# Kernel optimization log

Measured on AMD Instinct MI355X. Metric: run time of the kernel, lower is better.

Reference implementation:

```python
import jax, jax.numpy as jnp
import numpy as np

QC = 13        # quantum_channel
NQ = 12        # qubits per patch circuit
LAYERS12 = 3   # num_layer for FQConv ansatz
LAYERS4 = 4    # layers for the 4-qubit basic ansatz
GROUPS = 10
DIM = 40       # 3*QC + 1 channels
B = 1024
TDIM = 128
EPS = 1e-6     # flax GroupNorm default epsilon
TWO_PI = 2.0 * float(np.pi)


def _take2(s, ax):
    return jnp.take(s, 0, axis=ax), jnp.take(s, 1, axis=ax)


def init_state(n, N):
    # |0...0> state, shape (N, 2, 2, ..., 2); wire w lives on axis w+1
    s = jnp.zeros((N, 2 ** n), jnp.complex64).at[:, 0].set(1.0)
    return s.reshape((N,) + (2,) * n)


def apply_rx(state, theta, w):
    # RX(theta) = [[c, -i s], [-i s, c]], c=cos(theta/2), s=sin(theta/2)
    ax = w + 1
    theta = jnp.asarray(theta, jnp.float32)
    c = jnp.cos(0.5 * theta)
    s = jnp.sin(0.5 * theta)
    if theta.ndim > 0:  # per-sample angles (data embedding)
        sh = (-1,) + (1,) * (state.ndim - 2)
        c = c.reshape(sh)
        s = s.reshape(sh)
    c = c.astype(state.dtype)
    js = (1j * s).astype(state.dtype)
    s0, s1 = _take2(state, ax)
    return jnp.stack([c * s0 - js * s1, c * s1 - js * s0], axis=ax)


def apply_cnot(state, c, t):
    ca = c + 1
    ta = t + 1 if t < c else t  # target axis inside the control=1 slice
    s0, s1 = _take2(state, ca)
    return jnp.stack([s0, jnp.flip(s1, axis=ta)], axis=ca)


def apply_crz(state, theta, c, t):
    # CRZ = diag(1, 1, e^{-i theta/2}, e^{+i theta/2})
    ca = c + 1
    ta = t + 1 if t < c else t
    s0, s1 = _take2(state, ca)
    t0, t1 = _take2(s1, ta)
    em = jnp.exp(-0.5j * theta).astype(state.dtype)
    ep = jnp.exp(0.5j * theta).astype(state.dtype)
    s1 = jnp.stack([em * t0, ep * t1], axis=ta)
    return jnp.stack([s0, s1], axis=ca)


def apply_crx(state, theta, c, t):
    # controlled RX on target when control = 1
    ca = c + 1
    ta = t + 1 if t < c else t
    s0, s1 = _take2(state, ca)
    t0, t1 = _take2(s1, ta)
    ch = jnp.cos(0.5 * theta).astype(state.dtype)
    js = (1j * jnp.sin(0.5 * theta)).astype(state.dtype)
    s1 = jnp.stack([ch * t0 - js * t1, ch * t1 - js * t0], axis=ta)
    return jnp.stack([s0, s1], axis=ca)


def expvals_z(state, n):
    # <Z_w> = P(bit_w = 0) - P(bit_w = 1)
    p = jnp.real(state * jnp.conj(state))
    zs = []
    for w in range(n):
        axes = tuple(a for a in range(1, n + 1) if a != w + 1)
        q = p.sum(axis=axes)  # (N, 2)
        zs.append(q[:, 0] - q[:, 1])
    return jnp.stack(zs, axis=-1)  # (N, n)


def fqconv_layer(state, th):
    # zip(range(11,-1,-4), range(12)) -> i in (11,7,3), j in (0,1,2)
    for j, i in enumerate((11, 7, 3)):
        w1 = [i - 3, i - 2, i - 1, i] + [(i + k) % NQ for k in (1, 2, 3, 4)]
        tj = th[8 * j: 8 * (j + 1)]
        for bi, bj in zip(range(3, -1, -1), range(4)):  # block_C: CRZ
            state = apply_crz(state, TWO_PI * tj[bj], w1[bi + 4], w1[bi])
        for bi, bj in zip(range(3, -1, -1), range(4)):  # block_D: CRX
            state = apply_crx(state, TWO_PI * tj[4 + bj], w1[bi + 4], w1[bi])
    return state


def circuit12(x, theta):
    # x: (N, 12) angles; theta: (72,)
    state = init_state(NQ, x.shape[0])
    for w in range(NQ):  # AngleEmbedding, rotation='X'
        state = apply_rx(state, x[:, w], w)
    for l in range(LAYERS12):
        state = fqconv_layer(state, theta[24 * l: 24 * (l + 1)])
    return expvals_z(state, NQ)


def circuit4(x, theta):
    # Basic_ansatz, 4 qubits, 4 layers, 4 params/layer
    state = init_state(4, x.shape[0])
    for w in range(4):
        state = apply_rx(state, x[:, w], w)
    for l in range(LAYERS4):
        for w in range(4):
            state = apply_rx(state, theta[4 * l + w], w)
        for w in range(3):
            state = apply_cnot(state, w, w + 1)
        state = apply_cnot(state, 3, 0)
    return expvals_z(state, 4)


def run12_all(y, params, circ):
    # scan over the QC per-channel circuits (same structure, different params)
    def body(carry, xp):
        yy, th = xp
        return carry, circ(yy, th)
    _, zs = jax.lax.scan(body, None, (y, params))
    return zs  # (QC, N, 12)


def group_norm(h, scale, bias):
    Bn, H, W, C = h.shape
    g = h.reshape(Bn, H, W, GROUPS, C // GROUPS)
    mu = g.mean(axis=(1, 2, 4), keepdims=True)
    var = g.var(axis=(1, 2, 4), keepdims=True)
    g = (g - mu) * jax.lax.rsqrt(var + EPS)
    return g.reshape(Bn, H, W, C) * scale + bias


def forward(x, time_emb, qparams12, qparams4, gn0_scale, gn0_bias,
            gn1_scale, gn1_bias, time_w, time_b, circ12=circuit12):
    Bn = x.shape[0]

    def qpass(inp, p12_block):
        # per-channel 12-qubit circuits on 2x2x3 patches
        y = jnp.stack([inp[..., 3 * i:3 * (i + 1)].reshape(-1, 12) for i in range(QC)], 0)
        z = run12_all(y, p12_block, circ12)                      # (QC, Bn, 12)
        h1 = jnp.moveaxis(z.reshape(QC, Bn, 2, 2, 3), 0, -2).reshape(Bn, 2, 2, 3 * QC)
        # NOTE: faithful to the source, BOTH passes use circuit/params[-2]
        h4 = circuit4(inp[..., 3 * QC:].reshape(-1, 4), qparams4[0]).reshape(Bn, 2, 2, 1)
        return jnp.concatenate([h1, h4], axis=-1)                 # (Bn, 2, 2, 40)

    h = qpass(x, qparams12[:QC])
    h = group_norm(h, gn0_scale, gn0_bias)
    t = jax.nn.swish(time_emb) @ time_w + time_b                  # (Bn, 2*DIM)
    scale, shift = jnp.split(t[:, None, None, :], 2, axis=-1)
    h = jax.nn.swish(h * (1.0 + scale) + shift)
    h = qpass(h, qparams12[QC:])
    h = jax.nn.swish(group_norm(h, gn1_scale, gn1_bias))
    return x + h  # C == dim, so no res_conv


def setup_inputs() -> dict:
    key = jax.random.key(0)
    ks = jax.random.split(key, 5)
    return {
        "x": jax.random.normal(ks[0], (B, 2, 2, DIM), jnp.float32),
        "time_emb": jax.random.normal(ks[1], (B, TDIM), jnp.float32),
        "qparams12": jax.random.uniform(ks[2], (2 * QC, 24 * LAYERS12), jnp.float32),
        "qparams4": jax.random.uniform(ks[3], (2, 16), jnp.float32),
        "gn0_scale": jnp.ones((DIM,), jnp.float32),
        "gn0_bias": jnp.zeros((DIM,), jnp.float32),
        "gn1_scale": jnp.ones((DIM,), jnp.float32),
        "gn1_bias": jnp.zeros((DIM,), jnp.float32),
        "time_w": jax.random.normal(ks[4], (TDIM, 2 * DIM), jnp.float32) * (TDIM ** -0.5),
        "time_b": jnp.zeros((2 * DIM,), jnp.float32),
    }


def reference(x, time_emb, qparams12, qparams4, gn0_scale, gn0_bias,
              gn1_scale, gn1_bias, time_w, time_b):
    return forward(x, time_emb, qparams12, qparams4, gn0_scale, gn0_bias,
                   gn1_scale, gn1_bias, time_w, time_b)
```

## Files before the change

### kernel.cpp

```cpp
#include <hip/hip_runtime.h>
#include <math.h>


#define PI_F 3.14159265358979323846f

typedef float f2 __attribute__((ext_vector_type(2)));

__device__ __forceinline__ f2 shfl2(f2 v, int mask)
{
    f2 r;
    r[0] = __shfl_xor(v[0], mask, 64);
    r[1] = __shfl_xor(v[1], mask, 64);
    return r;
}

template<int CB>
__device__ __forceinline__ void crz_ctrlj(float cg, float ss, f2* R, f2* I)
{
#pragma unroll
    for (int j = 0; j < 16; ++j) {
        if (!((j >> CB) & 1)) continue;
        f2 r = R[j], im = I[j];
        R[j] = cg * r - ss * im;
        I[j] = cg * im + ss * r;
    }
}

__device__ __forceinline__ void crz_pairhi_t4(float cg, float sg, f2* R, f2* I)
{
    const f2 mrv = {1.0f, cg};
#pragma unroll
    for (int j = 0; j < 16; ++j) {
        f2 miv = {0.0f, (j & 8) ? sg : -sg};
        f2 r = R[j], im = I[j];
        R[j] = mrv * r - miv * im;
        I[j] = mrv * im + miv * r;
    }
}

__device__ __forceinline__ void crx_pair(float cg, float sg, f2* R, f2* I)
{
#pragma unroll
    for (int j = 0; j < 16; ++j) {
        f2 r = R[j], im = I[j];
        f2 rs = __builtin_shufflevector(r, r, 1, 0);
        f2 is = __builtin_shufflevector(im, im, 1, 0);
        R[j] = cg * r + sg * is;
        I[j] = cg * im - sg * rs;
    }
}

template<int M>
__device__ __forceinline__ void crx_elem(float cg, float sg, f2* R, f2* I)
{
#pragma unroll
    for (int j = 0; j < 16; ++j) {
        if (j & M) continue;
        const int p = j | M;
        f2 r0 = R[j], i0 = I[j], r1 = R[p], i1 = I[p];
        R[j] = cg * r0 + sg * i1;  I[j] = cg * i0 - sg * r1;
        R[p] = cg * r1 + sg * i0;  I[p] = cg * i1 - sg * r0;
    }
}

__device__ __forceinline__ void crx_pairhi_t4(float cg, float sg, f2* R, f2* I)
{
    const f2 cgv = {1.0f, cg};
    const f2 sgv = {0.0f, sg};
#pragma unroll
    for (int j = 0; j < 8; ++j) {
        const int p = j + 8;
        f2 r0 = R[j], i0 = I[j], r1 = R[p], i1 = I[p];
        R[j] = cgv * r0 + sgv * i1;  I[j] = cgv * i0 - sgv * r1;
        R[p] = cgv * r1 + sgv * i0;  I[p] = cgv * i1 - sgv * r0;
    }
}

template<int CB, int LT>
__device__ __forceinline__ void crx_shj(float cg, float sg, f2* R, f2* I)
{
#pragma unroll
    for (int j = 0; j < 16; ++j) {
        if (!((j >> CB) & 1)) continue;
        f2 br = shfl2(R[j], 1 << LT);
        f2 bi = shfl2(I[j], 1 << LT);
        f2 r = R[j], im = I[j];
        R[j] = cg * r + sg * bi;
        I[j] = cg * im - sg * br;
    }
}

template<int LT>
__device__ __forceinline__ void crx_perm_allv(float cg, float sg, f2* R, f2* I)
{
#pragma unroll
    for (int j = 0; j < 16; ++j) {
        float a0 = R[j][0], b0 = I[j][0];
        float a1 = R[j][1], b1 = I[j][1];
        if constexpr (LT == 4) {
            asm("v_permlane16_swap_b32 %0, %1\n\t"
                "v_permlane16_swap_b32 %1, %0" : "+v"(a0), "+v"(b0));
            asm("v_permlane16_swap_b32 %0, %1\n\t"
                "v_permlane16_swap_b32 %1, %0" : "+v"(a1), "+v"(b1));
        } else {
            asm("v_permlane32_swap_b32 %0, %1\n\t"
                "v_permlane32_swap_b32 %1, %0" : "+v"(a0), "+v"(b0));
            asm("v_permlane32_swap_b32 %0, %1\n\t"
                "v_permlane32_swap_b32 %1, %0" : "+v"(a1), "+v"(b1));
        }
        f2 A = {a0, a1}, Bv = {b0, b1};
        f2 r = R[j], im = I[j];
        R[j] = cg * r + sg * A;
        I[j] = cg * im - sg * Bv;
    }
}

__device__ __forceinline__ void crz_g0_fused(const float* a, f2* R, f2* I,
                                             int lane, int wv)
{
    float gr[4], gi[4];
#pragma unroll
    for (int m = 0; m < 4; ++m) {
        bool cb = (m < 3) ? ((lane >> (3 + m)) & 1) : (wv != 0);
        gr[m] = cb ? a[2 * m]     : 1.0f;
        gi[m] = cb ? a[2 * m + 1] : 0.0f;
    }
    float u0 = gr[1] * gr[0], v0 = gi[1] * gi[0];
    float w0 = gr[1] * gi[0], z0 = gi[1] * gr[0];
    float p01r[2] = { u0 - v0, u0 + v0 };
    float p01i[2] = { -(w0 + z0), w0 - z0 };
    float u1 = gr[3] * gr[2], v1 = gi[3] * gi[2];
    float w1 = gr[3] * gi[2], z1 = gi[3] * gr[2];
    float p23r[2] = { u1 - v1, u1 + v1 };
    float p23i[2] = { -(w1 + z1), w1 - z1 };

    float Mr[8], Mi[8];
#pragma unroll
    for (int t = 0; t < 8; ++t) {
        const int t10 = t & 3, t2 = (t >> 2) & 1;
        float br = (t10 == 0 || t10 == 3) ? p01r[0] : p01r[1];
        float bi = (t10 == 0) ? p01i[0] : (t10 == 1) ? p01i[1]
                 : (t10 == 2) ? -p01i[1] : -p01i[0];
        float ar = p23r[t2], ai = p23i[t2];
        Mr[t] = ar * br - ai * bi;
        Mi[t] = ar * bi + ai * br;
    }
#pragma unroll
    for (int j = 0; j < 16; ++j) {
        const int jj = j & 7;
        f2 mr, mi;
        if (jj < 4) {
            mr = f2{ Mr[2 * jj],      Mr[2 * jj + 1] };
            mi = f2{ Mi[2 * jj],      Mi[2 * jj + 1] };
        } else {
            mr = f2{ Mr[15 - 2 * jj], Mr[14 - 2 * jj] };
            mi = f2{ -Mi[15 - 2 * jj], -Mi[14 - 2 * jj] };
        }
        f2 r = R[j], im = I[j];
        R[j] = mr * r - mi * im;
        I[j] = mr * im + mi * r;
    }
}

__device__ __forceinline__ void crz_g2_fused(const float* a, f2* R, f2* I,
                                             int lane, int wv)
{
    float s0p = ((lane >> 3) & 1) ? a[1] : -a[1];
    bool cb1 = lane & 1;
    float sg1 = ((lane >> 4) & 1) ? a[3] : -a[3];
    float g1r = cb1 ? a[2] : 1.0f, g1i = cb1 ? sg1 : 0.0f;
    bool cb2 = (lane >> 1) & 1;
    float sg2 = ((lane >> 5) & 1) ? a[5] : -a[5];
    float g2r = cb2 ? a[4] : 1.0f, g2i = cb2 ? sg2 : 0.0f;
    bool cb3 = (lane >> 2) & 1;
    float sg3 = wv ? a[7] : -a[7];
    float g3r = cb3 ? a[6] : 1.0f, g3i = cb3 ? sg3 : 0.0f;
    float t12r = g1r * g2r - g1i * g2i, t12i = g1r * g2i + g1i * g2r;
    float Sr  = t12r * g3r - t12i * g3i;
    float Si_ = t12r * g3i + t12i * g3r;
    float T1r = Sr * a[0] - Si_ * s0p;
    float T1i = Sr * s0p + Si_ * a[0];
#pragma unroll
    for (int j = 0; j < 16; ++j) {
        float tr = (j & 8) ? T1r : Sr;
        float ti = (j & 8) ? T1i : Si_;
        f2 r = R[j], im = I[j];
        R[j] = tr * r - ti * im;
        I[j] = tr * im + ti * r;
    }
}

__global__ void __launch_bounds__(256, 2)
qpass12_kernel(const float* __restrict__ inp, const float* __restrict__ cs,
               float* __restrict__ outp)
{
    __shared__ f2 xbufv[2 * 2 * 32 * 33];
    float* xbuff = reinterpret_cast<float*>(xbufv);
    const int tid  = threadIdx.x;
    const int simL = tid >> 7;
    const int ts   = tid & 127;
    const int wv   = ts >> 6;
    const int lane = ts & 63;
    const int sim  = blockIdx.x * 2 + simL;
    const int ci = sim % 13;
    const int b  = sim / 13;
    const float* csc = cs + ci * 144;
    const int ibase = b * 160 + ci * 3;

    float cw[12], sw[12];
#pragma unroll
    for (int w = 0; w < 12; ++w) {
        float x = inp[ibase + (w / 3) * 40 + (w % 3)];
        __sincosf(0.5f * x, &sw[w], &cw[w]);
    }

    float pref = wv ? sw[0] : cw[0];
#pragma unroll
    for (int w = 1; w < 7; ++w)
        pref *= ((lane >> (6 - w)) & 1) ? sw[w] : cw[w];

    float fb[8], eb[4];
#pragma unroll
    for (int t = 0; t < 8; ++t)
        fb[t] = ((t & 1) ? sw[11] : cw[11]) * ((t & 2) ? sw[10] : cw[10]) *
                ((t & 4) ? sw[9] : cw[9]);
#pragma unroll
    for (int t = 0; t < 4; ++t)
        eb[t] = pref * ((t & 1) ? sw[8] : cw[8]) * ((t & 2) ? sw[7] : cw[7]);
    f2 fbv[4];
#pragma unroll
    for (int t = 0; t < 4; ++t)
        fbv[t] = f2{ fb[2 * t], fb[2 * t + 1] };

    const int pl = (__popc(lane) + wv) & 3;
    float oa = (pl == 0) ? 1.0f : (pl == 2) ? -1.0f : 0.0f;
    float ob = (pl == 1) ? -1.0f : (pl == 3) ? 1.0f : 0.0f;

    f2 R[16], I[16];
#pragma unroll
    for (int j = 0; j < 16; ++j) {
        f2 v2 = eb[j >> 2] * fbv[j & 3];
        const int q0 = ((j & 1) + ((j >> 1) & 1) + ((j >> 2) & 1) + ((j >> 3) & 1)) & 3;
        const int q1 = (q0 + 1) & 3;
        const float c0l = (q0 == 0) ? oa : (q0 == 1) ? ob : (q0 == 2) ? -oa : -ob;
        const float c1l = (q0 == 0) ? ob : (q0 == 1) ? -oa : (q0 == 2) ? -ob : oa;
        const float c0h = (q1 == 0) ? oa : (q1 == 1) ? ob : (q1 == 2) ? -oa : -ob;
        const float c1h = (q1 == 0) ? ob : (q1 == 1) ? -oa : (q1 == 2) ? -ob : oa;
        R[j] = f2{ v2[0] * c0l, v2[1] * c0h };
        I[j] = f2{ v2[0] * c1l, v2[1] * c1h };
    }

    const bool act = (lane >> 2) & 1;
    const int  ai  = ((lane >> 3) << 2) | (lane & 3);
    f2* xw = &xbufv[(((simL << 1) | wv) * 32 + ai) * 33];
    f2* xr = &xbufv[(((simL << 1) | (wv ^ 1)) * 32 + ai) * 33];

#pragma unroll 1
    for (int l = 0; l < 3; ++l) {
        const float* a = csc + l * 48;

        crz_g0_fused(a, R, I, lane, wv);
        { bool cb = (lane >> 3) & 1;
          crx_pair(cb ? a[ 8] : 1.0f, cb ? a[ 9] : 0.0f, R, I); }
        { bool cb = (lane >> 4) & 1;
          crx_elem<1>(cb ? a[10] : 1.0f, cb ? a[11] : 0.0f, R, I); }
        { bool cb = (lane >> 5) & 1;
          crx_elem<2>(cb ? a[12] : 1.0f, cb ? a[13] : 0.0f, R, I); }
        { bool cb = wv != 0;
          crx_elem<4>(cb ? a[14] : 1.0f, cb ? a[15] : 0.0f, R, I); }

        crz_pairhi_t4(a[16], a[17], R, I);
        { float ss = (lane & 1)        ? a[19] : -a[19]; crz_ctrlj<0>(a[18], ss, R, I); }
        { float ss = ((lane >> 1) & 1) ? a[21] : -a[21]; crz_ctrlj<1>(a[20], ss, R, I); }
        { float ss = ((lane >> 2) & 1) ? a[23] : -a[23]; crz_ctrlj<2>(a[22], ss, R, I); }
        crx_pairhi_t4(a[24], a[25], R, I);
        crx_shj<0, 0>(a[26], a[27], R, I);
        crx_shj<1, 1>(a[28], a[29], R, I);
        crx_shj<2, 2>(a[30], a[31], R, I);

        crz_g2_fused(a + 32, R, I, lane, wv);
        crx_shj<3, 3>(a[40], a[41], R, I);
        { bool cb = lane & 1;
          crx_perm_allv<4>(cb ? a[42] : 1.0f, cb ? a[43] : 0.0f, R, I); }
        { bool cb = (lane >> 1) & 1;
          crx_perm_allv<5>(cb ? a[44] : 1.0f, cb ? a[45] : 0.0f, R, I); }
        __syncthreads();
        if (act) {
#pragma unroll
            for (int j = 0; j < 16; ++j) {
                xw[j]      = R[j];
                xw[16 + j] = I[j];
            }
        }
        __syncthreads();
        if (act) {
            float cg = a[46], sg = a[47];
#pragma unroll
            for (int j = 0; j < 16; ++j) {
                f2 br = xr[j], bi = xr[16 + j];
                f2 r = R[j], im = I[j];
                R[j] = cg * r + sg * bi;
                I[j] = cg * im - sg * br;
            }
        }
    }

    f2 accT = {0.0f, 0.0f}, acc7 = {0.0f, 0.0f}, acc8 = {0.0f, 0.0f};
    f2 acc9 = {0.0f, 0.0f}, acc10 = {0.0f, 0.0f};
#pragma unroll
    for (int j = 0; j < 16; ++j) {
        f2 p = R[j] * R[j] + I[j] * I[j];
        accT += p;
        if (j & 8) acc7 -= p; else acc7 += p;
        if (j & 4) acc8 -= p; else acc8 += p;
        if (j & 2) acc9 -= p; else acc9 += p;
        if (j & 1) acc10 -= p; else acc10 += p;
    }
    float total = accT[0] + accT[1];
    float v12[12];
    v12[0] = wv ? -total : total;
#pragma unroll
    for (int w = 1; w < 7; ++w)
        v12[w] = ((lane >> (6 - w)) & 1) ? -total : total;
    v12[7]  = acc7[0] + acc7[1];
    v12[8]  = acc8[0] + acc8[1];
    v12[9]  = acc9[0] + acc9[1];
    v12[10] = acc10[0] + acc10[1];
    v12[11] = accT[0] - accT[1];

#pragma unroll
    for (int w = 0; w < 12; ++w) {
#pragma unroll
        for (int off = 1; off < 64; off <<= 1)
            v12[w] += __shfl_xor(v12[w], off, 64);
    }
    __syncthreads();
    if (lane == 0) {
#pragma unroll
        for (int w = 0; w < 12; ++w)
            xbuff[((simL << 1) | wv) * 12 + w] = v12[w];
    }
    __syncthreads();
    if (ts < 12) {
        float z = xbuff[(simL << 1) * 12 + ts] +
                  xbuff[((simL << 1) | 1) * 12 + ts];
        outp[ibase + (ts / 3) * 40 + (ts % 3)] = z;
    }
}

__global__ void q4_kernel(const float* __restrict__ inp,
                          const float* __restrict__ cs4,
                          float* __restrict__ outp)
{
    int b = blockIdx.x * blockDim.x + threadIdx.x;
    if (b >= 1024) return;
    float cw[4], sw[4];
#pragma unroll
    for (int j = 0; j < 4; ++j) {
        float x = inp[(b * 4 + j) * 40 + 39];
        __sincosf(0.5f * x, &sw[j], &cw[j]);
    }
    float sr[16], si[16];
#pragma unroll
    for (int k = 0; k < 16; ++k) {
        float v = 1.0f;
#pragma unroll
        for (int j = 0; j < 4; ++j)
            v *= ((k >> (3 - j)) & 1) ? sw[j] : cw[j];
        int ph = __popc(k) & 3;
        sr[k] = (ph == 0) ? v : (ph == 2) ? -v : 0.0f;
        si[k] = (ph == 1) ? -v : (ph == 3) ? v : 0.0f;
    }
#pragma unroll
    for (int l = 0; l < 4; ++l) {
#pragma unroll
        for (int w = 0; w < 4; ++w) {
            float cg = cs4[2 * (4 * l + w)], sg = cs4[2 * (4 * l + w) + 1];
            const int m = 1 << (3 - w);
#pragma unroll
            for (int k = 0; k < 16; ++k) {
                if (k & m) continue;
                int p2 = k | m;
                float r0 = sr[k], i0 = si[k], r1 = sr[p2], i1 = si[p2];
                sr[k]  = cg * r0 + sg * i1;  si[k]  = cg * i0 - sg * r1;
                sr[p2] = cg * r1 + sg * i0;  si[p2] = cg * i1 - sg * r0;
            }
        }
#pragma unroll
        for (int e = 0; e < 4; ++e) {
            const int cq = e, tq = (e + 1) & 3;
            const int pcb = 1 << (3 - cq), ptb = 1 << (3 - tq);
#pragma unroll
            for (int k = 0; k < 16; ++k) {
                if (!(k & pcb)) continue;
                if (k & ptb) continue;
                int p2 = k | ptb;
                float tr = sr[k], ti = si[k];
                sr[k] = sr[p2]; si[k] = si[p2];
                sr[p2] = tr;    si[p2] = ti;
            }
        }
    }
    float p[16];
#pragma unroll
    for (int k = 0; k < 16; ++k) p[k] = sr[k] * sr[k] + si[k] * si[k];
#pragma unroll
    for (int j = 0; j < 4; ++j) {
        float z = 0.0f;
#pragma unroll
        for (int k = 0; k < 16; ++k)
            z += ((k >> (3 - j)) & 1) ? -p[k] : p[k];
        outp[(b * 4 + j) * 40 + 39] = z;
    }
}

__global__ void prep_kernel(const float* __restrict__ q12,
                            const float* __restrict__ q4,
                            float* __restrict__ cs12,
                            float* __restrict__ cs4)
{
    int idx = blockIdx.x * 256 + threadIdx.x;
    if (idx < 26 * 72) {
        float s, c;
        sincosf(PI_F * q12[idx], &s, &c);
        cs12[2 * idx]     = c;
        cs12[2 * idx + 1] = s;
    }
    if (idx < 16) {
        float s, c;
        sincosf(0.5f * q4[idx], &s, &c);
        cs4[2 * idx]     = c;
        cs4[2 * idx + 1] = s;
    }
}

__global__ void tmlp_kernel(const float* __restrict__ emb,
                            const float* __restrict__ W,
                            const float* __restrict__ bias,
                            float* __restrict__ t)
{
    __shared__ float se[128];
    int b = blockIdx.x, tid = threadIdx.x;
    float e = emb[b * 128 + tid];
    se[tid] = e / (1.0f + __expf(-e));
    __syncthreads();
    if (tid < 80) {
        float acc = bias[tid];
        for (int k = 0; k < 128; ++k) acc += se[k] * W[k * 80 + tid];
        t[b * 80 + tid] = acc;
    }
}

__global__ void gn0_kernel(const float* __restrict__ h, const float* __restrict__ t,
                           const float* __restrict__ sc, const float* __restrict__ bi,
                           float* __restrict__ outp)
{
    __shared__ float v[160];
    __shared__ float mu[10], rstd[10];
    int b = blockIdx.x, tid = threadIdx.x;
    if (tid < 160) v[tid] = h[b * 160 + tid];
    __syncthreads();
    if (tid < 10) {
        float s1 = 0.0f, s2 = 0.0f;
#pragma unroll
        for (int sp = 0; sp < 4; ++sp)
#pragma unroll
            for (int k = 0; k < 4; ++k) {
                float x = v[sp * 40 + tid * 4 + k];
                s1 += x; s2 += x * x;
            }
        float m = s1 * (1.0f / 16.0f);
        float var = s2 * (1.0f / 16.0f) - m * m;
        mu[tid] = m; rstd[tid] = rsqrtf(var + 1e-6f);
    }
    __syncthreads();
    if (tid < 160) {
        int ch = tid % 40;
        int g = ch >> 2;
        float hn = (v[tid] - mu[g]) * rstd[g] * sc[ch] + bi[ch];
        float scale = t[b * 80 + ch], shift = t[b * 80 + 40 + ch];
        float z = hn * (1.0f + scale) + shift;
        outp[b * 160 + tid] = z / (1.0f + __expf(-z));
    }
}

__global__ void gn1_kernel(const float* __restrict__ h, const float* __restrict__ x,
                           const float* __restrict__ sc, const float* __restrict__ bi,
                           float* __restrict__ outp)
{
    __shared__ float v[160];
    __shared__ float mu[10], rstd[10];
    int b = blockIdx.x, tid = threadIdx.x;
    if (tid < 160) v[tid] = h[b * 160 + tid];
    __syncthreads();
    if (tid < 10) {
        float s1 = 0.0f, s2 = 0.0f;
#pragma unroll
        for (int sp = 0; sp < 4; ++sp)
#pragma unroll
            for (int k = 0; k < 4; ++k) {
                float xx = v[sp * 40 + tid * 4 + k];
                s1 += xx; s2 += xx * xx;
            }
        float m = s1 * (1.0f / 16.0f);
        float var = s2 * (1.0f / 16.0f) - m * m;
        mu[tid] = m; rstd[tid] = rsqrtf(var + 1e-6f);
    }
    __syncthreads();
    if (tid < 160) {
        int ch = tid % 40;
        int g = ch >> 2;
        float hn = (v[tid] - mu[g]) * rstd[g] * sc[ch] + bi[ch];
        float sws = hn / (1.0f + __expf(-hn));
        outp[b * 160 + tid] = x[b * 160 + tid] + sws;
    }
}

extern "C" void kernel_launch(void* const* d_in, const int* in_sizes, int n_in,
                              void* d_out, int out_size, void* d_ws, size_t ws_size,
                              hipStream_t stream)
{
    const float* x    = (const float*)d_in[0];
    const float* temb = (const float*)d_in[1];
    const float* q12  = (const float*)d_in[2];
    const float* q4   = (const float*)d_in[3];
    const float* gn0s = (const float*)d_in[4];
    const float* gn0b = (const float*)d_in[5];
    const float* gn1s = (const float*)d_in[6];
    const float* gn1b = (const float*)d_in[7];
    const float* tw   = (const float*)d_in[8];
    const float* tb   = (const float*)d_in[9];
    float* out = (float*)d_out;

    float* ws   = (float*)d_ws;
    float* cs12 = ws;
    float* cs4  = cs12 + 3744;
    float* tbuf = cs4 + 32;
    float* A    = tbuf + 81920;
    float* Bf   = A + 163840;

    prep_kernel<<<8, 256, 0, stream>>>(q12, q4, cs12, cs4);
    tmlp_kernel<<<1024, 128, 0, stream>>>(temb, tw, tb, tbuf);

    qpass12_kernel<<<6656, 256, 0, stream>>>(x, cs12, A);
    q4_kernel<<<16, 64, 0, stream>>>(x, cs4, A);
    gn0_kernel<<<1024, 160, 0, stream>>>(A, tbuf, gn0s, gn0b, Bf);

    qpass12_kernel<<<6656, 256, 0, stream>>>(Bf, cs12 + 13 * 144, A);
    q4_kernel<<<16, 64, 0, stream>>>(Bf, cs4, A);
    gn1_kernel<<<1024, 160, 0, stream>>>(A, x, gn1s, gn1b, out);
}
```

Baseline: 643.2 us.

## Spread each 12-qubit statevector over four wavefronts instead of two

```diff
diff --git a/kernel.cpp b/kernel.cpp
--- a/kernel.cpp
+++ b/kernel.cpp
@@ -14,34 +14,58 @@
     return r;
 }
 
-template<int CB>
-__device__ __forceinline__ void crz_ctrlj(float cg, float ss, f2* R, f2* I)
-{
-#pragma unroll
-    for (int j = 0; j < 16; ++j) {
-        if (!((j >> CB) & 1)) continue;
-        f2 r = R[j], im = I[j];
-        R[j] = cg * r - ss * im;
-        I[j] = cg * im + ss * r;
-    }
-}
-
-__device__ __forceinline__ void crz_pairhi_t4(float cg, float sg, f2* R, f2* I)
-{
-    const f2 mrv = {1.0f, cg};
-#pragma unroll
-    for (int j = 0; j < 16; ++j) {
-        f2 miv = {0.0f, (j & 8) ? sg : -sg};
-        f2 r = R[j], im = I[j];
-        R[j] = mrv * r - miv * im;
-        I[j] = mrv * im + miv * r;
+__device__ __forceinline__ void crz_g0_fused(const float* a, f2* R, f2* I,
+                                             int lane, int wq)
+{
+    float gr[4], gi[4];
+#pragma unroll
+    for (int m = 0; m < 4; ++m) {
+        bool cb;
+        if      (m == 0) cb = (lane >> 4) & 1;
+        else if (m == 1) cb = (lane >> 5) & 1;
+        else if (m == 2) cb = wq & 1;
+        else             cb = (wq >> 1) & 1;
+        gr[m] = cb ? a[2 * m]     : 1.0f;
+        gi[m] = cb ? a[2 * m + 1] : 0.0f;
+    }
+    float u0 = gr[1] * gr[0], v0 = gi[1] * gi[0];
+    float w0 = gr[1] * gi[0], z0 = gi[1] * gr[0];
+    float p01r[2] = { u0 - v0, u0 + v0 };
+    float p01i[2] = { -(w0 + z0), w0 - z0 };
+    float u1 = gr[3] * gr[2], v1 = gi[3] * gi[2];
+    float w1 = gr[3] * gi[2], z1 = gi[3] * gr[2];
+    float p23r[2] = { u1 - v1, u1 + v1 };
+    float p23i[2] = { -(w1 + z1), w1 - z1 };
+
+#pragma unroll
+    for (int j = 0; j < 8; ++j) {
+        const int ta  = (j < 4) ? 2 * j     : 15 - 2 * j;
+        const int tb  = (j < 4) ? 2 * j + 1 : 14 - 2 * j;
+        const float sgn = (j < 4) ? 1.0f : -1.0f;
+        const int a10 = ta & 3, a2 = (ta >> 2) & 1;
+        float bar = (a10 == 0 || a10 == 3) ? p01r[0] : p01r[1];
+        float bai = (a10 == 0) ? p01i[0] : (a10 == 1) ? p01i[1]
+                  : (a10 == 2) ? -p01i[1] : -p01i[0];
+        float m0r = p23r[a2] * bar - p23i[a2] * bai;
+        float m0i = p23r[a2] * bai + p23i[a2] * bar;
+        const int b10 = tb & 3, b2 = (tb >> 2) & 1;
+        float bbr = (b10 == 0 || b10 == 3) ? p01r[0] : p01r[1];
+        float bbi = (b10 == 0) ? p01i[0] : (b10 == 1) ? p01i[1]
+                  : (b10 == 2) ? -p01i[1] : -p01i[0];
+        float m1r = p23r[b2] * bbr - p23i[b2] * bbi;
+        float m1i = p23r[b2] * bbi + p23i[b2] * bbr;
+        f2 mr = { m0r, m1r };
+        f2 mi = { sgn * m0i, sgn * m1i };
+        f2 r = R[j], im = I[j];
+        R[j] = mr * r - mi * im;
+        I[j] = mr * im + mi * r;
     }
 }
 
 __device__ __forceinline__ void crx_pair(float cg, float sg, f2* R, f2* I)
 {
 #pragma unroll
-    for (int j = 0; j < 16; ++j) {
+    for (int j = 0; j < 8; ++j) {
         f2 r = R[j], im = I[j];
         f2 rs = __builtin_shufflevector(r, r, 1, 0);
         f2 is = __builtin_shufflevector(im, im, 1, 0);
@@ -54,7 +78,7 @@
 __device__ __forceinline__ void crx_elem(float cg, float sg, f2* R, f2* I)
 {
 #pragma unroll
-    for (int j = 0; j < 16; ++j) {
+    for (int j = 0; j < 8; ++j) {
         if (j & M) continue;
         const int p = j | M;
         f2 r0 = R[j], i0 = I[j], r1 = R[p], i1 = I[p];
@@ -63,41 +87,93 @@
     }
 }
 
-__device__ __forceinline__ void crx_pairhi_t4(float cg, float sg, f2* R, f2* I)
+__device__ __forceinline__ void crz_e(float cg, float ss, f2* R, f2* I)
+{
+    const f2 mrv = {1.0f, cg};
+    const f2 miv = {0.0f, ss};
+#pragma unroll
+    for (int j = 0; j < 8; ++j) {
+        f2 r = R[j], im = I[j];
+        R[j] = mrv * r - miv * im;
+        I[j] = mrv * im + miv * r;
+    }
+}
+
+template<int CB>
+__device__ __forceinline__ void crz_ctrlj(float cg, float ss, f2* R, f2* I)
+{
+#pragma unroll
+    for (int j = 0; j < 8; ++j) {
+        if (!((j >> CB) & 1)) continue;
+        f2 r = R[j], im = I[j];
+        R[j] = cg * r - ss * im;
+        I[j] = cg * im + ss * r;
+    }
+}
+
+__device__ __forceinline__ void crx_sh_e(float cg, float sg, f2* R, f2* I)
 {
     const f2 cgv = {1.0f, cg};
     const f2 sgv = {0.0f, sg};
 #pragma unroll
     for (int j = 0; j < 8; ++j) {
-        const int p = j + 8;
-        f2 r0 = R[j], i0 = I[j], r1 = R[p], i1 = I[p];
-        R[j] = cgv * r0 + sgv * i1;  I[j] = cgv * i0 - sgv * r1;
-        R[p] = cgv * r1 + sgv * i0;  I[p] = cgv * i1 - sgv * r0;
-    }
-}
-
-template<int CB, int LT>
+        f2 br = shfl2(R[j], 1);
+        f2 bi = shfl2(I[j], 1);
+        f2 r = R[j], im = I[j];
+        R[j] = cgv * r + sgv * bi;
+        I[j] = cgv * im - sgv * br;
+    }
+}
+
+template<int CB, int MASK>
 __device__ __forceinline__ void crx_shj(float cg, float sg, f2* R, f2* I)
 {
 #pragma unroll
-    for (int j = 0; j < 16; ++j) {
+    for (int j = 0; j < 8; ++j) {
         if (!((j >> CB) & 1)) continue;
-        f2 br = shfl2(R[j], 1 << LT);
-        f2 bi = shfl2(I[j], 1 << LT);
+        f2 br = shfl2(R[j], MASK);
+        f2 bi = shfl2(I[j], MASK);
         f2 r = R[j], im = I[j];
         R[j] = cg * r + sg * bi;
         I[j] = cg * im - sg * br;
     }
 }
 
-template<int LT>
-__device__ __forceinline__ void crx_perm_allv(float cg, float sg, f2* R, f2* I)
-{
-#pragma unroll
-    for (int j = 0; j < 16; ++j) {
+__device__ __forceinline__ void crz_g2_fused(const float* a, f2* R, f2* I,
+                                             int lane, int wq)
+{
+    float s0 = ((lane >> 4) & 1) ? a[1] : -a[1];
+    bool  c0 = lane & 1;
+    float f0r = c0 ? a[0] : 1.0f, f0i = c0 ? s0 : 0.0f;
+    float s1 = ((lane >> 5) & 1) ? a[3] : -a[3];
+    bool  c1 = (lane >> 1) & 1;
+    float f1r = c1 ? a[2] : 1.0f, f1i = c1 ? s1 : 0.0f;
+    float s2 = (wq & 1) ? a[5] : -a[5];
+    bool  c2 = (lane >> 2) & 1;
+    float f2r = c2 ? a[4] : 1.0f, f2i = c2 ? s2 : 0.0f;
+    float s3 = ((wq >> 1) & 1) ? a[7] : -a[7];
+    bool  c3 = (lane >> 3) & 1;
+    float f3r = c3 ? a[6] : 1.0f, f3i = c3 ? s3 : 0.0f;
+    float t01r = f0r * f1r - f0i * f1i, t01i = f0r * f1i + f0i * f1r;
+    float t23r = f2r * f3r - f2i * f3i, t23i = f2r * f3i + f2i * f3r;
+    float Pr = t01r * t23r - t01i * t23i;
+    float Pi = t01r * t23i + t01i * t23r;
+#pragma unroll
+    for (int j = 0; j < 8; ++j) {
+        f2 r = R[j], im = I[j];
+        R[j] = Pr * r - Pi * im;
+        I[j] = Pr * im + Pi * r;
+    }
+}
+
+template<int MASK>
+__device__ __forceinline__ void crx_perm(float cg, float sg, f2* R, f2* I)
+{
+#pragma unroll
+    for (int j = 0; j < 8; ++j) {
         float a0 = R[j][0], b0 = I[j][0];
         float a1 = R[j][1], b1 = I[j][1];
-        if constexpr (LT == 4) {
+        if constexpr (MASK == 16) {
             asm("v_permlane16_swap_b32 %0, %1\n\t"
                 "v_permlane16_swap_b32 %1, %0" : "+v"(a0), "+v"(b0));
             asm("v_permlane16_swap_b32 %0, %1\n\t"
@@ -115,93 +191,16 @@
     }
 }
 
-__device__ __forceinline__ void crz_g0_fused(const float* a, f2* R, f2* I,
-                                             int lane, int wv)
-{
-    float gr[4], gi[4];
-#pragma unroll
-    for (int m = 0; m < 4; ++m) {
-        bool cb = (m < 3) ? ((lane >> (3 + m)) & 1) : (wv != 0);
-        gr[m] = cb ? a[2 * m]     : 1.0f;
-        gi[m] = cb ? a[2 * m + 1] : 0.0f;
-    }
-    float u0 = gr[1] * gr[0], v0 = gi[1] * gi[0];
-    float w0 = gr[1] * gi[0], z0 = gi[1] * gr[0];
-    float p01r[2] = { u0 - v0, u0 + v0 };
-    float p01i[2] = { -(w0 + z0), w0 - z0 };
-    float u1 = gr[3] * gr[2], v1 = gi[3] * gi[2];
-    float w1 = gr[3] * gi[2], z1 = gi[3] * gr[2];
-    float p23r[2] = { u1 - v1, u1 + v1 };
-    float p23i[2] = { -(w1 + z1), w1 - z1 };
-
-    float Mr[8], Mi[8];
-#pragma unroll
-    for (int t = 0; t < 8; ++t) {
-        const int t10 = t & 3, t2 = (t >> 2) & 1;
-        float br = (t10 == 0 || t10 == 3) ? p01r[0] : p01r[1];
-        float bi = (t10 == 0) ? p01i[0] : (t10 == 1) ? p01i[1]
-                 : (t10 == 2) ? -p01i[1] : -p01i[0];
-        float ar = p23r[t2], ai = p23i[t2];
-        Mr[t] = ar * br - ai * bi;
-        Mi[t] = ar * bi + ai * br;
-    }
-#pragma unroll
-    for (int j = 0; j < 16; ++j) {
-        const int jj = j & 7;
-        f2 mr, mi;
-        if (jj < 4) {
-            mr = f2{ Mr[2 * jj],      Mr[2 * jj + 1] };
-            mi = f2{ Mi[2 * jj],      Mi[2 * jj + 1] };
-        } else {
-            mr = f2{ Mr[15 - 2 * jj], Mr[14 - 2 * jj] };
-            mi = f2{ -Mi[15 - 2 * jj], -Mi[14 - 2 * jj] };
-        }
-        f2 r = R[j], im = I[j];
-        R[j] = mr * r - mi * im;
-        I[j] = mr * im + mi * r;
-    }
-}
-
-__device__ __forceinline__ void crz_g2_fused(const float* a, f2* R, f2* I,
-                                             int lane, int wv)
-{
-    float s0p = ((lane >> 3) & 1) ? a[1] : -a[1];
-    bool cb1 = lane & 1;
-    float sg1 = ((lane >> 4) & 1) ? a[3] : -a[3];
-    float g1r = cb1 ? a[2] : 1.0f, g1i = cb1 ? sg1 : 0.0f;
-    bool cb2 = (lane >> 1) & 1;
-    float sg2 = ((lane >> 5) & 1) ? a[5] : -a[5];
-    float g2r = cb2 ? a[4] : 1.0f, g2i = cb2 ? sg2 : 0.0f;
-    bool cb3 = (lane >> 2) & 1;
-    float sg3 = wv ? a[7] : -a[7];
-    float g3r = cb3 ? a[6] : 1.0f, g3i = cb3 ? sg3 : 0.0f;
-    float t12r = g1r * g2r - g1i * g2i, t12i = g1r * g2i + g1i * g2r;
-    float Sr  = t12r * g3r - t12i * g3i;
-    float Si_ = t12r * g3i + t12i * g3r;
-    float T1r = Sr * a[0] - Si_ * s0p;
-    float T1i = Sr * s0p + Si_ * a[0];
-#pragma unroll
-    for (int j = 0; j < 16; ++j) {
-        float tr = (j & 8) ? T1r : Sr;
-        float ti = (j & 8) ? T1i : Si_;
-        f2 r = R[j], im = I[j];
-        R[j] = tr * r - ti * im;
-        I[j] = tr * im + ti * r;
-    }
-}
-
-__global__ void __launch_bounds__(256, 2)
+__global__ void __launch_bounds__(256, 4)
 qpass12_kernel(const float* __restrict__ inp, const float* __restrict__ cs,
                float* __restrict__ outp)
 {
-    __shared__ f2 xbufv[2 * 2 * 32 * 33];
+    __shared__ f2 xbufv[4 * 32 * 17];
     float* xbuff = reinterpret_cast<float*>(xbufv);
-    const int tid  = threadIdx.x;
-    const int simL = tid >> 7;
-    const int ts   = tid & 127;
-    const int wv   = ts >> 6;
+    const int ts   = threadIdx.x;
+    const int wq   = ts >> 6;
     const int lane = ts & 63;
-    const int sim  = blockIdx.x * 2 + simL;
+    const int sim  = blockIdx.x;
     const int ci = sim % 13;
     const int b  = sim / 13;
     const float* csc = cs + ci * 144;
@@ -214,33 +213,22 @@
         __sincosf(0.5f * x, &sw[w], &cw[w]);
     }
 
-    float pref = wv ? sw[0] : cw[0];
-#pragma unroll
-    for (int w = 1; w < 7; ++w)
-        pref *= ((lane >> (6 - w)) & 1) ? sw[w] : cw[w];
-
-    float fb[8], eb[4];
-#pragma unroll
-    for (int t = 0; t < 8; ++t)
-        fb[t] = ((t & 1) ? sw[11] : cw[11]) * ((t & 2) ? sw[10] : cw[10]) *
-                ((t & 4) ? sw[9] : cw[9]);
-#pragma unroll
-    for (int t = 0; t < 4; ++t)
-        eb[t] = pref * ((t & 1) ? sw[8] : cw[8]) * ((t & 2) ? sw[7] : cw[7]);
-    f2 fbv[4];
-#pragma unroll
-    for (int t = 0; t < 4; ++t)
-        fbv[t] = f2{ fb[2 * t], fb[2 * t + 1] };
-
-    const int pl = (__popc(lane) + wv) & 3;
+    float pref = ((wq >> 1) ? sw[0] : cw[0]) * ((wq & 1) ? sw[1] : cw[1]);
+#pragma unroll
+    for (int w = 2; w < 8; ++w)
+        pref *= ((lane >> (7 - w)) & 1) ? sw[w] : cw[w];
+
+    const int pl = (__popc(lane) + __popc(wq)) & 3;
     float oa = (pl == 0) ? 1.0f : (pl == 2) ? -1.0f : 0.0f;
     float ob = (pl == 1) ? -1.0f : (pl == 3) ? 1.0f : 0.0f;
 
-    f2 R[16], I[16];
-#pragma unroll
-    for (int j = 0; j < 16; ++j) {
-        f2 v2 = eb[j >> 2] * fbv[j & 3];
-        const int q0 = ((j & 1) + ((j >> 1) & 1) + ((j >> 2) & 1) + ((j >> 3) & 1)) & 3;
+    f2 R[8], I[8];
+#pragma unroll
+    for (int j = 0; j < 8; ++j) {
+        float base = pref * ((j & 4) ? sw[8] : cw[8]) *
+                     ((j & 2) ? sw[9] : cw[9]) * ((j & 1) ? sw[10] : cw[10]);
+        f2 v2 = { base * cw[11], base * sw[11] };
+        const int q0 = __popc(j) & 3;
         const int q1 = (q0 + 1) & 3;
         const float c0l = (q0 == 0) ? oa : (q0 == 1) ? ob : (q0 == 2) ? -oa : -ob;
         const float c1l = (q0 == 0) ? ob : (q0 == 1) ? -oa : (q0 == 2) ? -ob : oa;
@@ -250,79 +238,104 @@
         I[j] = f2{ v2[0] * c1l, v2[1] * c1h };
     }
 
-    const bool act = (lane >> 2) & 1;
-    const int  ai  = ((lane >> 3) << 2) | (lane & 3);
-    f2* xw = &xbufv[(((simL << 1) | wv) * 32 + ai) * 33];
-    f2* xr = &xbufv[(((simL << 1) | (wv ^ 1)) * 32 + ai) * 33];
+    const bool act2 = (lane >> 2) & 1;
+    const bool act3 = (lane >> 3) & 1;
+    const int ai2 = ((lane >> 3) << 2) | (lane & 3);
+    const int ai3 = ((lane >> 4) << 3) | (lane & 7);
+    f2* xw2 = &xbufv[(wq * 32 + ai2) * 17];
+    f2* xr2 = &xbufv[((wq ^ 1) * 32 + ai2) * 17];
+    f2* xw3 = &xbufv[(wq * 32 + ai3) * 17];
+    f2* xr3 = &xbufv[((wq ^ 2) * 32 + ai3) * 17];
 
 #pragma unroll 1
     for (int l = 0; l < 3; ++l) {
         const float* a = csc + l * 48;
 
-        crz_g0_fused(a, R, I, lane, wv);
-        { bool cb = (lane >> 3) & 1;
+        crz_g0_fused(a, R, I, lane, wq);
+        { bool cb = (lane >> 4) & 1;
           crx_pair(cb ? a[ 8] : 1.0f, cb ? a[ 9] : 0.0f, R, I); }
-        { bool cb = (lane >> 4) & 1;
+        { bool cb = (lane >> 5) & 1;
           crx_elem<1>(cb ? a[10] : 1.0f, cb ? a[11] : 0.0f, R, I); }
-        { bool cb = (lane >> 5) & 1;
+        { bool cb = wq & 1;
           crx_elem<2>(cb ? a[12] : 1.0f, cb ? a[13] : 0.0f, R, I); }
-        { bool cb = wv != 0;
+        { bool cb = (wq >> 1) & 1;
           crx_elem<4>(cb ? a[14] : 1.0f, cb ? a[15] : 0.0f, R, I); }
 
-        crz_pairhi_t4(a[16], a[17], R, I);
-        { float ss = (lane & 1)        ? a[19] : -a[19]; crz_ctrlj<0>(a[18], ss, R, I); }
-        { float ss = ((lane >> 1) & 1) ? a[21] : -a[21]; crz_ctrlj<1>(a[20], ss, R, I); }
-        { float ss = ((lane >> 2) & 1) ? a[23] : -a[23]; crz_ctrlj<2>(a[22], ss, R, I); }
-        crx_pairhi_t4(a[24], a[25], R, I);
-        crx_shj<0, 0>(a[26], a[27], R, I);
-        crx_shj<1, 1>(a[28], a[29], R, I);
-        crx_shj<2, 2>(a[30], a[31], R, I);
-
-        crz_g2_fused(a + 32, R, I, lane, wv);
-        crx_shj<3, 3>(a[40], a[41], R, I);
+        { float ss = (lane & 1) ? a[17] : -a[17];
+          crz_e(a[16], ss, R, I); }
+        { float ss = ((lane >> 1) & 1) ? a[19] : -a[19];
+          crz_ctrlj<0>(a[18], ss, R, I); }
+        { float ss = ((lane >> 2) & 1) ? a[21] : -a[21];
+          crz_ctrlj<1>(a[20], ss, R, I); }
+        { float ss = ((lane >> 3) & 1) ? a[23] : -a[23];
+          crz_ctrlj<2>(a[22], ss, R, I); }
+        crx_sh_e(a[24], a[25], R, I);
+        crx_shj<0, 2>(a[26], a[27], R, I);
+        crx_shj<1, 4>(a[28], a[29], R, I);
+        crx_shj<2, 8>(a[30], a[31], R, I);
+
+        crz_g2_fused(a + 32, R, I, lane, wq);
         { bool cb = lane & 1;
-          crx_perm_allv<4>(cb ? a[42] : 1.0f, cb ? a[43] : 0.0f, R, I); }
+          crx_perm<16>(cb ? a[40] : 1.0f, cb ? a[41] : 0.0f, R, I); }
         { bool cb = (lane >> 1) & 1;
-          crx_perm_allv<5>(cb ? a[44] : 1.0f, cb ? a[45] : 0.0f, R, I); }
+          crx_perm<32>(cb ? a[42] : 1.0f, cb ? a[43] : 0.0f, R, I); }
         __syncthreads();
-        if (act) {
-#pragma unroll
-            for (int j = 0; j < 16; ++j) {
-                xw[j]      = R[j];
-                xw[16 + j] = I[j];
+        if (act2) {
+#pragma unroll
+            for (int j = 0; j < 8; ++j) {
+                xw2[j]     = R[j];
+                xw2[8 + j] = I[j];
             }
         }
         __syncthreads();
-        if (act) {
-            float cg = a[46], sg = a[47];
-#pragma unroll
-            for (int j = 0; j < 16; ++j) {
-                f2 br = xr[j], bi = xr[16 + j];
+        if (act2) {
+            float cg = a[44], sg = a[45];
+#pragma unroll
+            for (int j = 0; j < 8; ++j) {
+                f2 br = xr2[j], bi = xr2[8 + j];
                 f2 r = R[j], im = I[j];
                 R[j] = cg * r + sg * bi;
                 I[j] = cg * im - sg * br;
             }
         }
-    }
-
-    f2 accT = {0.0f, 0.0f}, acc7 = {0.0f, 0.0f}, acc8 = {0.0f, 0.0f};
+        __syncthreads();
+        if (act3) {
+#pragma unroll
+            for (int j = 0; j < 8; ++j) {
+                xw3[j]     = R[j];
+                xw3[8 + j] = I[j];
+            }
+        }
+        __syncthreads();
+        if (act3) {
+            float cg = a[46], sg = a[47];
+#pragma unroll
+            for (int j = 0; j < 8; ++j) {
+                f2 br = xr3[j], bi = xr3[8 + j];
+                f2 r = R[j], im = I[j];
+                R[j] = cg * r + sg * bi;
+                I[j] = cg * im - sg * br;
+            }
+        }
+    }
+
+    f2 accT = {0.0f, 0.0f}, acc8 = {0.0f, 0.0f};
     f2 acc9 = {0.0f, 0.0f}, acc10 = {0.0f, 0.0f};
 #pragma unroll
-    for (int j = 0; j < 16; ++j) {
+    for (int j = 0; j < 8; ++j) {
         f2 p = R[j] * R[j] + I[j] * I[j];
         accT += p;
-        if (j & 8) acc7 -= p; else acc7 += p;
         if (j & 4) acc8 -= p; else acc8 += p;
         if (j & 2) acc9 -= p; else acc9 += p;
         if (j & 1) acc10 -= p; else acc10 += p;
     }
     float total = accT[0] + accT[1];
     float v12[12];
-    v12[0] = wv ? -total : total;
-#pragma unroll
-    for (int w = 1; w < 7; ++w)
-        v12[w] = ((lane >> (6 - w)) & 1) ? -total : total;
-    v12[7]  = acc7[0] + acc7[1];
+    v12[0] = (wq >> 1) ? -total : total;
+    v12[1] = (wq & 1) ? -total : total;
+#pragma unroll
+    for (int w = 2; w < 8; ++w)
+        v12[w] = ((lane >> (7 - w)) & 1) ? -total : total;
     v12[8]  = acc8[0] + acc8[1];
     v12[9]  = acc9[0] + acc9[1];
     v12[10] = acc10[0] + acc10[1];
@@ -338,12 +351,11 @@
     if (lane == 0) {
 #pragma unroll
         for (int w = 0; w < 12; ++w)
-            xbuff[((simL << 1) | wv) * 12 + w] = v12[w];
+            xbuff[wq * 12 + w] = v12[w];
     }
     __syncthreads();
     if (ts < 12) {
-        float z = xbuff[(simL << 1) * 12 + ts] +
-                  xbuff[((simL << 1) | 1) * 12 + ts];
+        float z = xbuff[ts] + xbuff[12 + ts] + xbuff[24 + ts] + xbuff[36 + ts];
         outp[ibase + (ts / 3) * 40 + (ts % 3)] = z;
     }
 }
@@ -542,11 +554,11 @@
     prep_kernel<<<8, 256, 0, stream>>>(q12, q4, cs12, cs4);
     tmlp_kernel<<<1024, 128, 0, stream>>>(temb, tw, tb, tbuf);
 
-    qpass12_kernel<<<6656, 256, 0, stream>>>(x, cs12, A);
+    qpass12_kernel<<<13312, 256, 0, stream>>>(x, cs12, A);
     q4_kernel<<<16, 64, 0, stream>>>(x, cs4, A);
     gn0_kernel<<<1024, 160, 0, stream>>>(A, tbuf, gn0s, gn0b, Bf);
 
-    qpass12_kernel<<<6656, 256, 0, stream>>>(Bf, cs12 + 13 * 144, A);
+    qpass12_kernel<<<13312, 256, 0, stream>>>(Bf, cs12 + 13 * 144, A);
     q4_kernel<<<16, 64, 0, stream>>>(Bf, cs4, A);
     gn1_kernel<<<1024, 160, 0, stream>>>(A, x, gn1s, gn1b, out);
 }
```

Result: no change. 650.6 us (+1.2%).
